# Optimization experiments

Measured on AMD Instinct MI355X. Metric: run time of the kernel, lower is better.

Reference implementation:

```python
import jax, jax.numpy as jnp
import numpy as np

B, T, D = 2, 2048, 1024
H = 4
KD = int(D * 0.5)      # total key dim = 512
VD = int(D * 1.0)      # total value dim = 1024
DK, DV = KD // H, VD // H  # per-head: 128, 256
CHUNK = 64
LOW_RANK = 16          # gate_low_rank_dim
NORMALIZER = 16.0      # gate_logit_normalizer
EPS = 1e-6


def setup_inputs() -> dict:
    key = jax.random.key(0)
    ks = jax.random.split(key, 10)
    def w(k, shape):
        return jax.random.normal(k, shape, jnp.float32) / np.sqrt(shape[0]).astype(np.float32)
    return {
        "x": jax.random.normal(ks[0], (B, T, D), jnp.float32),
        "Wq": w(ks[1], (D, KD)),
        "Wk": w(ks[2], (D, KD)),
        "Wv": w(ks[3], (D, VD)),
        "Wg": w(ks[4], (D, VD)),          # output gate projection
        "Wgk1": w(ks[5], (D, LOW_RANK)),  # low-rank gate proj (no bias)
        "Wgk2": w(ks[6], (LOW_RANK, KD)),
        "bgk2": jax.random.normal(ks[7], (KD,), jnp.float32) * 0.1,
        "gnorm_w": jnp.ones((DV,), jnp.float32),  # FusedRMSNormSwishGate weight
        "Wo": w(ks[8], (VD, D)),
    }


def reference(x, Wq, Wk, Wv, Wg, Wgk1, Wgk2, bgk2, gnorm_w, Wo):
    scale = DK ** -0.5
    NC = T // CHUNK
    # [B,T,d] -> [NC,B,H,C,d_head]
    to_heads = lambda a, d: a.reshape(B, NC, CHUNK, H, d).transpose(1, 0, 3, 2, 4)
    q = to_heads(x @ Wq, DK)
    k = to_heads(x @ Wk, DK)
    v = to_heads(x @ Wv, DV)
    # per-key log decay gate: logsigmoid(low-rank proj) / normalizer
    gk = jax.nn.log_sigmoid((x @ Wgk1) @ Wgk2 + bgk2) / NORMALIZER
    G = jnp.cumsum(to_heads(gk, DK), axis=3)  # inclusive cumsum within chunk

    def chunk_step(S, inp):
        k_c, v_c, G_c = inp                       # [B,H,C,DK],[B,H,C,DV],[B,H,C,DK]
        G_last = G_c[:, :, -1, :]                 # [B,H,DK] total chunk decay
        k_bar = k_c * jnp.exp(G_last[:, :, None, :] - G_c)  # decay pos->chunk end
        S_new = jnp.exp(G_last)[..., None] * S + jnp.einsum('bhck,bhcv->bhkv', k_bar, v_c)
        return S_new, S                           # emit state at chunk START

    S0 = jnp.zeros((B, H, DK, DV), x.dtype)
    _, S_prev = jax.lax.scan(chunk_step, S0, (k, v, G))  # [NC,B,H,DK,DV]

    qg = q * jnp.exp(G) * scale                   # decay-scaled queries
    o_inter = jnp.einsum('nbhck,nbhkv->nbhcv', qg, S_prev)
    kg = k * jnp.exp(-G)
    A = jnp.einsum('nbhik,nbhjk->nbhij', qg, kg)  # intra-chunk scores
    A = jnp.where(jnp.tril(jnp.ones((CHUNK, CHUNK), bool)), A, 0.0)
    o = o_inter + jnp.einsum('nbhij,nbhjv->nbhiv', A, v)  # [NC,B,H,C,DV]
    o = o.transpose(1, 0, 3, 2, 4).reshape(B, T, H, DV)

    # fused gated RMSNorm: rmsnorm(o)*weight * swish(g), then output proj
    g = (x @ Wg).reshape(B, T, H, DV)
    o = o * jax.lax.rsqrt(jnp.mean(o * o, axis=-1, keepdims=True) + EPS) * gnorm_w
    o = o * (g * jax.nn.sigmoid(g))
    return o.reshape(B, T, VD) @ Wo
```

## Files before the change

### kernel.cpp

```cpp
#include <hip/hip_runtime.h>
#include <hip/hip_bf16.h>

#define BDIM 2
#define TDIM 2048
#define DDIM 1024
#define HH 4
#define KD 512
#define VD 1024
#define DK 128
#define DV 256
#define NC 32
#define CHUNKC 64
#define MTOT (BDIM*TDIM)
#define QKG 1536
#define VGN 2048
#define STRIDE_ST ((size_t)BDIM*HH*DK*DV)

typedef __bf16 bf16x8 __attribute__((ext_vector_type(8)));
typedef float  f32x4  __attribute__((ext_vector_type(4)));
typedef __hip_bfloat16 hbf;

__device__ __forceinline__ void async_copy16(const void* g, void* l) {
  __builtin_amdgcn_global_load_lds(
      (const __attribute__((address_space(1))) void*)g,
      (__attribute__((address_space(3))) void*)l, 16, 0, 0);
}

__global__ void cast_bf16_kernel(const float* __restrict__ src, hbf* __restrict__ dst) {
  int t = blockIdx.x*256 + threadIdx.x;
  float4 v = ((const float4*)src)[t];
  union { hbf h[4]; uint2 u; } o;
  o.h[0] = __float2bfloat16(v.x); o.h[1] = __float2bfloat16(v.y);
  o.h[2] = __float2bfloat16(v.z); o.h[3] = __float2bfloat16(v.w);
  ((uint2*)dst)[t] = o.u;
}

__global__ void transpose_cast_kernel(const float* __restrict__ W, hbf* __restrict__ Wt,
                                      int K, int N) {
  __shared__ float tile[32][33];
  const int bx = blockIdx.x, by = blockIdx.y;
  const int tx = threadIdx.x & 31, ty = threadIdx.x >> 5;
  #pragma unroll
  for (int r = ty; r < 32; r += 8)
    tile[r][tx] = W[(size_t)(by*32 + r)*N + bx*32 + tx];
  __syncthreads();
  #pragma unroll
  for (int r = ty; r < 32; r += 8)
    Wt[(size_t)(bx*32 + r)*K + by*32 + tx] = __float2bfloat16(tile[tx][r]);
}

__global__ void wcomp_kernel(const float* __restrict__ W1, const float* __restrict__ W2,
                             hbf* __restrict__ Wct) {
  int idx = blockIdx.x*256 + threadIdx.x;
  int k = idx & 1023, n = idx >> 10;
  float s = 0.f;
  #pragma unroll
  for (int r = 0; r < 16; ++r) s += W1[k*16 + r] * W2[r*KD + n];
  Wct[(size_t)n*DDIM + k] = __float2bfloat16(s);
}

__global__ __launch_bounds__(256) void gemm_bt(const hbf* __restrict__ A,
                                               const hbf* __restrict__ Bt,
                                               float* __restrict__ C,
                                               int M, int N, int K) {
  __shared__ hbf As[128][32];
  __shared__ hbf Bs[128][32];
  const int t = threadIdx.x;
  const int w = t >> 6, l = t & 63;
  const int lr = l >> 2, lc = (l & 3)*8;
  const int lane16 = l & 15, quad = l >> 4;
  const int row0 = blockIdx.y*128, col0 = blockIdx.x*128;
  const int mb = (w >> 1)*64, nb = (w & 1)*64;

  const hbf* ga = A  + (size_t)(row0 + w*32 + lr)*K + lc;
  const hbf* gb = Bt + (size_t)(col0 + w*32 + lr)*K + lc;
  hbf* la0 = &As[w*32][0];      hbf* la1 = &As[w*32 + 16][0];
  hbf* lb0 = &Bs[w*32][0];      hbf* lb1 = &Bs[w*32 + 16][0];
  const size_t rstep = (size_t)16*K;

  f32x4 acc[4][4] = {};
  for (int k0 = 0; k0 < K; k0 += 32) {
    async_copy16(ga,         la0);
    async_copy16(ga + rstep, la1);
    async_copy16(gb,         lb0);
    async_copy16(gb + rstep, lb1);
    ga += 32; gb += 32;
    __syncthreads();
    bf16x8 af[4], bfr[4];
    #pragma unroll
    for (int i = 0; i < 4; ++i)
      af[i] = *(const bf16x8*)&As[mb + i*16 + lane16][quad*8];
    #pragma unroll
    for (int j = 0; j < 4; ++j)
      bfr[j] = *(const bf16x8*)&Bs[nb + j*16 + lane16][quad*8];
    #pragma unroll
    for (int i = 0; i < 4; ++i)
      #pragma unroll
      for (int j = 0; j < 4; ++j)
        acc[i][j] = __builtin_amdgcn_mfma_f32_16x16x32_bf16(af[i], bfr[j], acc[i][j], 0, 0, 0);
    __syncthreads();
  }
  #pragma unroll
  for (int i = 0; i < 4; ++i)
    #pragma unroll
    for (int j = 0; j < 4; ++j)
      #pragma unroll
      for (int r = 0; r < 4; ++r) {
        int m = row0 + mb + i*16 + quad*4 + r;
        int n = col0 + nb + j*16 + lane16;
        C[(size_t)m*N + n] = acc[i][j][r];
      }
}

__global__ __launch_bounds__(256) void gkcumsum_kernel(float* __restrict__ qkg,
                                                       const float* __restrict__ bias) {
  __shared__ float buf[CHUNKC][128];
  const int cs = blockIdx.x & 3;
  const int nc = (blockIdx.x >> 2) & 31;
  const int b  = blockIdx.x >> 7;
  const int t = threadIdx.x;
  const int bc = b*TDIM + nc*CHUNKC;
  const int col0 = cs*128;
  #pragma unroll
  for (int i = 0; i < 32; ++i) {
    int idx = t + 256*i;
    int c = idx >> 7, col = idx & 127;
    float s = qkg[(size_t)(bc + c)*QKG + 1024 + col0 + col] + bias[col0 + col];
    float ls = fminf(s, 0.f) - log1pf(expf(-fabsf(s)));
    buf[c][col] = ls * (1.0f/16.0f);
  }
  __syncthreads();
  if (t < 128) {
    float acc = 0.f;
    #pragma unroll
    for (int c = 0; c < CHUNKC; ++c) {
      acc += buf[c][t];
      buf[c][t] = acc;
    }
  }
  __syncthreads();
  #pragma unroll
  for (int i = 0; i < 32; ++i) {
    int idx = t + 256*i;
    int c = idx >> 7, col = idx & 127;
    qkg[(size_t)(bc + c)*QKG + 1024 + col0 + col] = buf[c][col];
  }
}

__global__ __launch_bounds__(256) void state_chunk_kernel(const float* __restrict__ qkg,
                                                          const float* __restrict__ vgb,
                                                          float* __restrict__ U,
                                                          float* __restrict__ dec) {
  const int bh = blockIdx.x & 7;
  const int nc = blockIdx.x >> 3;
  const int b = bh >> 2, h = bh & 3;
  const int t = threadIdx.x;
  const int w = t >> 6, l = t & 63;
  const int lane16 = l & 15, quad = l >> 4;
  __shared__ hbf kbarT[DK][72];
  __shared__ hbf vT[DV][72];
  __shared__ float glast[DK];
  const int bc = b*TDIM + nc*CHUNKC;
  if (t < DK) {
    float gl = qkg[(size_t)(bc + 63)*QKG + 1024 + h*DK + t];
    glast[t] = gl;
    dec[((size_t)nc*8 + bh)*DK + t] = expf(gl);
  }
  __syncthreads();
  #pragma unroll
  for (int i = 0; i < 32; ++i) {
    int idx = t + 256*i;
    int c = idx >> 7, kk = idx & 127;
    float g  = qkg[(size_t)(bc + c)*QKG + 1024 + h*DK + kk];
    float kv = qkg[(size_t)(bc + c)*QKG +  512 + h*DK + kk];
    kbarT[kk][c] = __float2bfloat16(kv * expf(glast[kk] - g));
  }
  #pragma unroll
  for (int i = 0; i < 64; ++i) {
    int idx = t + 256*i;
    int c = idx >> 8, col = idx & 255;
    vT[col][c] = __float2bfloat16(vgb[(size_t)(bc + c)*VGN + h*DV + col]);
  }
  __syncthreads();
  f32x4 acc[4][8] = {};
  #pragma unroll
  for (int kc = 0; kc < 2; ++kc) {
    bf16x8 av[4], bk[8];
    #pragma unroll
    for (int i = 0; i < 4; ++i)
      av[i] = *(const bf16x8*)&vT[w*64 + i*16 + lane16][kc*32 + quad*8];
    #pragma unroll
    for (int j = 0; j < 8; ++j)
      bk[j] = *(const bf16x8*)&kbarT[j*16 + lane16][kc*32 + quad*8];
    #pragma unroll
    for (int i = 0; i < 4; ++i)
      #pragma unroll
      for (int j = 0; j < 8; ++j)
        acc[i][j] = __builtin_amdgcn_mfma_f32_16x16x32_bf16(av[i], bk[j], acc[i][j], 0, 0, 0);
  }
  float* ub = U + ((size_t)nc*8 + bh)*((size_t)DK*DV);
  #pragma unroll
  for (int i = 0; i < 4; ++i)
    #pragma unroll
    for (int j = 0; j < 8; ++j)
      #pragma unroll
      for (int r = 0; r < 4; ++r) {
        int v = w*64 + i*16 + quad*4 + r;
        int k = j*16 + lane16;
        ub[(size_t)v*DK + k] = acc[i][j][r];
      }
}

__global__ __launch_bounds__(256) void state_scan_kernel(const float* __restrict__ U,
                                                         const float* __restrict__ dec,
                                                         hbf* __restrict__ Spb) {
  const int e = blockIdx.x*256 + threadIdx.x;
  const int k = e & 127;
  const int bh = e >> 15;
  float S = 0.f;
  for (int nc = 0; nc < NC; ++nc) {
    float u = U[(size_t)nc*STRIDE_ST + e];
    Spb[(size_t)nc*STRIDE_ST + e] = __float2bfloat16(S);
    S = S * dec[((size_t)nc*8 + bh)*DK + k] + u;
  }
}

__global__ __launch_bounds__(256) void out_kernel(const float* __restrict__ qkg,
                                                  const float* __restrict__ vgb,
                                                  const hbf* __restrict__ Spb,
                                                  const float* __restrict__ gnw,
                                                  hbf* __restrict__ obf) {
  const int blk = blockIdx.x;
  const int h = blk & 3, b = (blk >> 2) & 1, nc = blk >> 3;
  const int t = threadIdx.x;
  const int w = t >> 6, l = t & 63;
  const int lane16 = l & 15, quad = l >> 4;

  __shared__ __align__(16) unsigned char smem[64768];
  hbf (*qgs)[136] = (hbf(*)[136])(smem);
  hbf (*Ald)[72]  = (hbf(*)[72]) (smem + 17408);
  hbf (*kgs)[136] = (hbf(*)[136])(smem + 26624);
  hbf (*vT)[72]   = (hbf(*)[72]) (smem + 26624);
  float* ssum     = (float*)     (smem + 63488);
  float* invb     = (float*)     (smem + 64512);

  const float scale = 0.088388347648318447f;
  const int bc = b*TDIM + nc*CHUNKC;

  #pragma unroll
  for (int i = 0; i < 32; ++i) {
    int idx = t + 256*i;
    int c = idx >> 7, kk = idx & 127;
    size_t rb = (size_t)(bc + c)*QKG + h*DK;
    float g = qkg[rb + 1024 + (0)] ;
    g = qkg[rb + 1024 + kk - h*DK + h*DK];
    g = qkg[(size_t)(bc + c)*QKG + 1024 + h*DK + kk];
    qgs[c][kk] = __float2bfloat16(qkg[(size_t)(bc + c)*QKG + h*DK + kk] * expf(g) * scale);
    kgs[c][kk] = __float2bfloat16(qkg[(size_t)(bc + c)*QKG + 512 + h*DK + kk] * expf(-g));
  }
  __syncthreads();

  f32x4 acc1[4] = {};
  #pragma unroll
  for (int kc = 0; kc < 4; ++kc) {
    bf16x8 af = *(const bf16x8*)&qgs[w*16 + lane16][kc*32 + quad*8];
    #pragma unroll
    for (int j = 0; j < 4; ++j) {
      bf16x8 bf = *(const bf16x8*)&kgs[j*16 + lane16][kc*32 + quad*8];
      acc1[j] = __builtin_amdgcn_mfma_f32_16x16x32_bf16(af, bf, acc1[j], 0, 0, 0);
    }
  }
  __syncthreads();

  #pragma unroll
  for (int j = 0; j < 4; ++j)
    #pragma unroll
    for (int r = 0; r < 4; ++r) {
      int cr = w*16 + quad*4 + r;
      int cc = j*16 + lane16;
      Ald[cr][cc] = __float2bfloat16(cc <= cr ? acc1[j][r] : 0.f);
    }
  #pragma unroll
  for (int i = 0; i < 64; ++i) {
    int e = t + 256*i;
    int c = e >> 8, col = e & 255;
    vT[col][c] = __float2bfloat16(vgb[(size_t)(bc + c)*VGN + h*DV + col]);
  }
  __syncthreads();

  const hbf* SpB = Spb + ((size_t)nc*8 + (b*HH + h))*((size_t)DK*DV);
  f32x4 acc[4][4] = {};
  #pragma unroll
  for (int kc = 0; kc < 4; ++kc) {
    bf16x8 af[4], bs[4];
    #pragma unroll
    for (int i = 0; i < 4; ++i)
      af[i] = *(const bf16x8*)&qgs[i*16 + lane16][kc*32 + quad*8];
    #pragma unroll
    for (int j = 0; j < 4; ++j) {
      int n = w*64 + j*16 + lane16;
      bs[j] = *(const bf16x8*)(SpB + (size_t)n*DK + kc*32 + quad*8);
    }
    #pragma unroll
    for (int i = 0; i < 4; ++i)
      #pragma unroll
      for (int j = 0; j < 4; ++j)
        acc[i][j] = __builtin_amdgcn_mfma_f32_16x16x32_bf16(af[i], bs[j], acc[i][j], 0, 0, 0);
  }
  #pragma unroll
  for (int kc = 0; kc < 2; ++kc) {
    bf16x8 aa[4], bv[4];
    #pragma unroll
    for (int i = 0; i < 4; ++i)
      aa[i] = *(const bf16x8*)&Ald[i*16 + lane16][kc*32 + quad*8];
    #pragma unroll
    for (int j = 0; j < 4; ++j)
      bv[j] = *(const bf16x8*)&vT[w*64 + j*16 + lane16][kc*32 + quad*8];
    #pragma unroll
    for (int i = 0; i < 4; ++i)
      #pragma unroll
      for (int j = 0; j < 4; ++j)
        acc[i][j] = __builtin_amdgcn_mfma_f32_16x16x32_bf16(aa[i], bv[j], acc[i][j], 0, 0, 0);
  }

  #pragma unroll
  for (int i = 0; i < 4; ++i)
    #pragma unroll
    for (int r = 0; r < 4; ++r) {
      float s = 0.f;
      #pragma unroll
      for (int j = 0; j < 4; ++j) s += acc[i][j][r]*acc[i][j][r];
      s += __shfl_xor(s, 1); s += __shfl_xor(s, 2);
      s += __shfl_xor(s, 4); s += __shfl_xor(s, 8);
      if (lane16 == 0) ssum[(i*16 + quad*4 + r)*4 + w] = s;
    }
  __syncthreads();
  if (t < 64) {
    float tot = ssum[t*4] + ssum[t*4+1] + ssum[t*4+2] + ssum[t*4+3];
    invb[t] = rsqrtf(tot * (1.0f/DV) + 1e-6f);
  }
  __syncthreads();
  float gnwv[4];
  #pragma unroll
  for (int j = 0; j < 4; ++j) gnwv[j] = gnw[w*64 + j*16 + lane16];
  #pragma unroll
  for (int i = 0; i < 4; ++i)
    #pragma unroll
    for (int r = 0; r < 4; ++r) {
      int m = i*16 + quad*4 + r;
      float inv = invb[m];
      size_t grow_ = (size_t)(bc + m)*VGN + 1024 + h*DV + w*64;
      size_t orow_ = (size_t)(bc + m)*VD + h*DV + w*64;
      #pragma unroll
      for (int j = 0; j < 4; ++j) {
        float gv = vgb[grow_ + j*16 + lane16];
        float sig = 1.f / (1.f + expf(-gv));
        float val = acc[i][j][r] * inv * gnwv[j];
        obf[orow_ + j*16 + lane16] = __float2bfloat16(val * (gv * sig));
      }
    }
}

extern "C" void kernel_launch(void* const* d_in, const int* in_sizes, int n_in,
                              void* d_out, int out_size, void* d_ws, size_t ws_size,
                              hipStream_t stream) {
  const float* x    = (const float*)d_in[0];
  const float* Wq   = (const float*)d_in[1];
  const float* Wk   = (const float*)d_in[2];
  const float* Wv   = (const float*)d_in[3];
  const float* Wg   = (const float*)d_in[4];
  const float* Wgk1 = (const float*)d_in[5];
  const float* Wgk2 = (const float*)d_in[6];
  const float* bgk2 = (const float*)d_in[7];
  const float* gnw  = (const float*)d_in[8];
  const float* Wo   = (const float*)d_in[9];
  float* out = (float*)d_out;

  float* ws  = (float*)d_ws;
  float* qkg = ws;
  float* vgb = qkg + (size_t)MTOT*QKG;
  float* U   = vgb + (size_t)MTOT*VGN;
  float* dec = U   + (size_t)NC*STRIDE_ST;
  float* bfr = dec + (size_t)NC*BDIM*HH*DK;
  hbf* xbf   = (hbf*)bfr;
  hbf* wtqkg = xbf   + (size_t)MTOT*DDIM;
  hbf* wtvg  = wtqkg + (size_t)QKG*DDIM;
  hbf* wto   = wtvg  + (size_t)VGN*DDIM;
  hbf* Spb   = wto   + (size_t)DDIM*DDIM;
  hbf* obf   = (hbf*)U;

  cast_bf16_kernel<<<MTOT*DDIM/4/256, 256, 0, stream>>>(x, xbf);
  transpose_cast_kernel<<<dim3(512/32, DDIM/32), 256, 0, stream>>>(Wq, wtqkg, DDIM, 512);
  transpose_cast_kernel<<<dim3(512/32, DDIM/32), 256, 0, stream>>>(Wk, wtqkg + (size_t)512*DDIM, DDIM, 512);
  wcomp_kernel<<<512*1024/256, 256, 0, stream>>>(Wgk1, Wgk2, wtqkg + (size_t)1024*DDIM);
  transpose_cast_kernel<<<dim3(1024/32, DDIM/32), 256, 0, stream>>>(Wv, wtvg, DDIM, 1024);
  transpose_cast_kernel<<<dim3(1024/32, DDIM/32), 256, 0, stream>>>(Wg, wtvg + (size_t)1024*DDIM, DDIM, 1024);
  transpose_cast_kernel<<<dim3(1024/32, DDIM/32), 256, 0, stream>>>(Wo, wto, DDIM, 1024);

  gemm_bt<<<dim3(QKG/128, MTOT/128), 256, 0, stream>>>(xbf, wtqkg, qkg, MTOT, QKG, DDIM);
  gemm_bt<<<dim3(VGN/128, MTOT/128), 256, 0, stream>>>(xbf, wtvg, vgb, MTOT, VGN, DDIM);

  gkcumsum_kernel<<<256, 256, 0, stream>>>(qkg, bgk2);
  state_chunk_kernel<<<NC*BDIM*HH, 256, 0, stream>>>(qkg, vgb, U, dec);
  state_scan_kernel<<<(int)(STRIDE_ST/256), 256, 0, stream>>>(U, dec, Spb);
  out_kernel<<<NC*BDIM*HH, 256, 0, stream>>>(qkg, vgb, Spb, gnw, obf);
  gemm_bt<<<dim3(DDIM/128, MTOT/128), 256, 0, stream>>>(obf, wto, out, MTOT, DDIM, DDIM);
}
```

Baseline: 262.8 us.

## Merge input projection GEMMs and store q/k/v/g and chunk states in bf16

The two input projection GEMMs are merged into one launch over a concatenated weight matrix. A templated epilogue routes q/k and v/g to bf16 buffers and keeps only the gate logits in fp32. The per-chunk state contributions U are also stored in bf16, and the scan kernel processes two elements per thread with vectorized loads. This cuts global memory traffic for the intermediates and removes one launch, at the cost of extra bf16 rounding of k/v and of the state increments before accumulation.

```diff
diff --git a/kernel.cpp b/kernel.cpp
--- a/kernel.cpp
+++ b/kernel.cpp
@@ -12,8 +12,7 @@
 #define NC 32
 #define CHUNKC 64
 #define MTOT (BDIM*TDIM)
-#define QKG 1536
-#define VGN 2048
+#define NALL 3584
 #define STRIDE_ST ((size_t)BDIM*HH*DK*DV)
 
 typedef __bf16 bf16x8 __attribute__((ext_vector_type(8)));
@@ -59,9 +58,12 @@
   Wct[(size_t)n*DDIM + k] = __float2bfloat16(s);
 }
 
+template <int MODE>
 __global__ __launch_bounds__(256) void gemm_bt(const hbf* __restrict__ A,
                                                const hbf* __restrict__ Bt,
-                                               float* __restrict__ C,
+                                               float* __restrict__ Cf,
+                                               hbf* __restrict__ Cq,
+                                               hbf* __restrict__ Cv,
                                                int M, int N, int K) {
   __shared__ hbf As[128][32];
   __shared__ hbf Bs[128][32];
@@ -108,11 +110,18 @@
       for (int r = 0; r < 4; ++r) {
         int m = row0 + mb + i*16 + quad*4 + r;
         int n = col0 + nb + j*16 + lane16;
-        C[(size_t)m*N + n] = acc[i][j][r];
+        float v = acc[i][j][r];
+        if (MODE == 0) {
+          Cf[(size_t)m*N + n] = v;
+        } else {
+          if (col0 < 1024)       Cq[(size_t)m*1024 + n] = __float2bfloat16(v);
+          else if (col0 < 1536)  Cf[(size_t)m*512  + n - 1024] = v;
+          else                   Cv[(size_t)m*2048 + n - 1536] = __float2bfloat16(v);
+        }
       }
 }
 
-__global__ __launch_bounds__(256) void gkcumsum_kernel(float* __restrict__ qkg,
+__global__ __launch_bounds__(256) void gkcumsum_kernel(float* __restrict__ Gb,
                                                        const float* __restrict__ bias) {
   __shared__ float buf[CHUNKC][128];
   const int cs = blockIdx.x & 3;
@@ -125,7 +134,7 @@
   for (int i = 0; i < 32; ++i) {
     int idx = t + 256*i;
     int c = idx >> 7, col = idx & 127;
-    float s = qkg[(size_t)(bc + c)*QKG + 1024 + col0 + col] + bias[col0 + col];
+    float s = Gb[(size_t)(bc + c)*KD + col0 + col] + bias[col0 + col];
     float ls = fminf(s, 0.f) - log1pf(expf(-fabsf(s)));
     buf[c][col] = ls * (1.0f/16.0f);
   }
@@ -143,13 +152,14 @@
   for (int i = 0; i < 32; ++i) {
     int idx = t + 256*i;
     int c = idx >> 7, col = idx & 127;
-    qkg[(size_t)(bc + c)*QKG + 1024 + col0 + col] = buf[c][col];
-  }
-}
-
-__global__ __launch_bounds__(256) void state_chunk_kernel(const float* __restrict__ qkg,
-                                                          const float* __restrict__ vgb,
-                                                          float* __restrict__ U,
+    Gb[(size_t)(bc + c)*KD + col0 + col] = buf[c][col];
+  }
+}
+
+__global__ __launch_bounds__(256) void state_chunk_kernel(const hbf* __restrict__ qkbf,
+                                                          const hbf* __restrict__ vgbf,
+                                                          const float* __restrict__ Gb,
+                                                          hbf* __restrict__ Ub,
                                                           float* __restrict__ dec) {
   const int bh = blockIdx.x & 7;
   const int nc = blockIdx.x >> 3;
@@ -162,7 +172,7 @@
   __shared__ float glast[DK];
   const int bc = b*TDIM + nc*CHUNKC;
   if (t < DK) {
-    float gl = qkg[(size_t)(bc + 63)*QKG + 1024 + h*DK + t];
+    float gl = Gb[(size_t)(bc + 63)*KD + h*DK + t];
     glast[t] = gl;
     dec[((size_t)nc*8 + bh)*DK + t] = expf(gl);
   }
@@ -171,15 +181,15 @@
   for (int i = 0; i < 32; ++i) {
     int idx = t + 256*i;
     int c = idx >> 7, kk = idx & 127;
-    float g  = qkg[(size_t)(bc + c)*QKG + 1024 + h*DK + kk];
-    float kv = qkg[(size_t)(bc + c)*QKG +  512 + h*DK + kk];
+    float g  = Gb[(size_t)(bc + c)*KD + h*DK + kk];
+    float kv = __bfloat162float(qkbf[(size_t)(bc + c)*1024 + 512 + h*DK + kk]);
     kbarT[kk][c] = __float2bfloat16(kv * expf(glast[kk] - g));
   }
   #pragma unroll
   for (int i = 0; i < 64; ++i) {
     int idx = t + 256*i;
     int c = idx >> 8, col = idx & 255;
-    vT[col][c] = __float2bfloat16(vgb[(size_t)(bc + c)*VGN + h*DV + col]);
+    vT[col][c] = vgbf[(size_t)(bc + c)*2048 + h*DV + col];
   }
   __syncthreads();
   f32x4 acc[4][8] = {};
@@ -198,7 +208,7 @@
       for (int j = 0; j < 8; ++j)
         acc[i][j] = __builtin_amdgcn_mfma_f32_16x16x32_bf16(av[i], bk[j], acc[i][j], 0, 0, 0);
   }
-  float* ub = U + ((size_t)nc*8 + bh)*((size_t)DK*DV);
+  hbf* ub = Ub + ((size_t)nc*8 + bh)*((size_t)DK*DV);
   #pragma unroll
   for (int i = 0; i < 4; ++i)
     #pragma unroll
@@ -207,26 +217,35 @@
       for (int r = 0; r < 4; ++r) {
         int v = w*64 + i*16 + quad*4 + r;
         int k = j*16 + lane16;
-        ub[(size_t)v*DK + k] = acc[i][j][r];
+        ub[(size_t)v*DK + k] = __float2bfloat16(acc[i][j][r]);
       }
 }
 
-__global__ __launch_bounds__(256) void state_scan_kernel(const float* __restrict__ U,
+__global__ __launch_bounds__(256) void state_scan_kernel(const hbf* __restrict__ Ub,
                                                          const float* __restrict__ dec,
                                                          hbf* __restrict__ Spb) {
-  const int e = blockIdx.x*256 + threadIdx.x;
-  const int k = e & 127;
-  const int bh = e >> 15;
-  float S = 0.f;
+  const int p = blockIdx.x*256 + threadIdx.x;
+  const size_t e = (size_t)p*2;
+  const int k = (int)(e & 127);
+  const int bh = (int)(e >> 15);
+  float S0 = 0.f, S1 = 0.f;
   for (int nc = 0; nc < NC; ++nc) {
-    float u = U[(size_t)nc*STRIDE_ST + e];
-    Spb[(size_t)nc*STRIDE_ST + e] = __float2bfloat16(S);
-    S = S * dec[((size_t)nc*8 + bh)*DK + k] + u;
-  }
-}
-
-__global__ __launch_bounds__(256) void out_kernel(const float* __restrict__ qkg,
-                                                  const float* __restrict__ vgb,
+    const size_t off = (size_t)nc*STRIDE_ST + e;
+    uint uu = *(const uint*)(Ub + off);
+    hbf u0 = *(const hbf*)&uu;
+    hbf u1 = *((const hbf*)&uu + 1);
+    union { hbf h[2]; uint u; } ov;
+    ov.h[0] = __float2bfloat16(S0); ov.h[1] = __float2bfloat16(S1);
+    *(uint*)(Spb + off) = ov.u;
+    float2 d = *(const float2*)(dec + ((size_t)nc*8 + bh)*DK + k);
+    S0 = S0 * d.x + __bfloat162float(u0);
+    S1 = S1 * d.y + __bfloat162float(u1);
+  }
+}
+
+__global__ __launch_bounds__(256) void out_kernel(const hbf* __restrict__ qkbf,
+                                                  const hbf* __restrict__ vgbf,
+                                                  const float* __restrict__ Gb,
                                                   const hbf* __restrict__ Spb,
                                                   const float* __restrict__ gnw,
                                                   hbf* __restrict__ obf) {
@@ -251,12 +270,11 @@
   for (int i = 0; i < 32; ++i) {
     int idx = t + 256*i;
     int c = idx >> 7, kk = idx & 127;
-    size_t rb = (size_t)(bc + c)*QKG + h*DK;
-    float g = qkg[rb + 1024 + (0)] ;
-    g = qkg[rb + 1024 + kk - h*DK + h*DK];
-    g = qkg[(size_t)(bc + c)*QKG + 1024 + h*DK + kk];
-    qgs[c][kk] = __float2bfloat16(qkg[(size_t)(bc + c)*QKG + h*DK + kk] * expf(g) * scale);
-    kgs[c][kk] = __float2bfloat16(qkg[(size_t)(bc + c)*QKG + 512 + h*DK + kk] * expf(-g));
+    float g = Gb[(size_t)(bc + c)*KD + h*DK + kk];
+    float qv = __bfloat162float(qkbf[(size_t)(bc + c)*1024 + h*DK + kk]);
+    float kv = __bfloat162float(qkbf[(size_t)(bc + c)*1024 + 512 + h*DK + kk]);
+    qgs[c][kk] = __float2bfloat16(qv * expf(g) * scale);
+    kgs[c][kk] = __float2bfloat16(kv * expf(-g));
   }
   __syncthreads();
 
@@ -284,7 +302,7 @@
   for (int i = 0; i < 64; ++i) {
     int e = t + 256*i;
     int c = e >> 8, col = e & 255;
-    vT[col][c] = __float2bfloat16(vgb[(size_t)(bc + c)*VGN + h*DV + col]);
+    vT[col][c] = vgbf[(size_t)(bc + c)*2048 + h*DV + col];
   }
   __syncthreads();
 
@@ -349,11 +367,11 @@
     for (int r = 0; r < 4; ++r) {
       int m = i*16 + quad*4 + r;
       float inv = invb[m];
-      size_t grow_ = (size_t)(bc + m)*VGN + 1024 + h*DV + w*64;
+      size_t grow_ = (size_t)(bc + m)*2048 + 1024 + h*DV + w*64;
       size_t orow_ = (size_t)(bc + m)*VD + h*DV + w*64;
       #pragma unroll
       for (int j = 0; j < 4; ++j) {
-        float gv = vgb[grow_ + j*16 + lane16];
+        float gv = __bfloat162float(vgbf[grow_ + j*16 + lane16]);
         float sig = 1.f / (1.f + expf(-gv));
         float val = acc[i][j][r] * inv * gnwv[j];
         obf[orow_ + j*16 + lane16] = __float2bfloat16(val * (gv * sig));
@@ -377,32 +395,30 @@
   float* out = (float*)d_out;
 
   float* ws  = (float*)d_ws;
-  float* qkg = ws;
-  float* vgb = qkg + (size_t)MTOT*QKG;
-  float* U   = vgb + (size_t)MTOT*VGN;
-  float* dec = U   + (size_t)NC*STRIDE_ST;
-  float* bfr = dec + (size_t)NC*BDIM*HH*DK;
-  hbf* xbf   = (hbf*)bfr;
-  hbf* wtqkg = xbf   + (size_t)MTOT*DDIM;
-  hbf* wtvg  = wtqkg + (size_t)QKG*DDIM;
-  hbf* wto   = wtvg  + (size_t)VGN*DDIM;
-  hbf* Spb   = wto   + (size_t)DDIM*DDIM;
-  hbf* obf   = (hbf*)U;
+  float* Gb  = ws;
+  float* dec = Gb  + (size_t)MTOT*KD;
+  hbf* xbf   = (hbf*)(dec + (size_t)NC*BDIM*HH*DK);
+  hbf* wtall = xbf   + (size_t)MTOT*DDIM;
+  hbf* wto   = wtall + (size_t)NALL*DDIM;
+  hbf* qkbf  = wto   + (size_t)DDIM*DDIM;
+  hbf* vgbf  = qkbf  + (size_t)MTOT*1024;
+  hbf* Ub    = vgbf  + (size_t)MTOT*2048;
+  hbf* Spb   = Ub    + (size_t)NC*STRIDE_ST;
+  hbf* obf   = Ub;
 
   cast_bf16_kernel<<<MTOT*DDIM/4/256, 256, 0, stream>>>(x, xbf);
-  transpose_cast_kernel<<<dim3(512/32, DDIM/32), 256, 0, stream>>>(Wq, wtqkg, DDIM, 512);
-  transpose_cast_kernel<<<dim3(512/32, DDIM/32), 256, 0, stream>>>(Wk, wtqkg + (size_t)512*DDIM, DDIM, 512);
-  wcomp_kernel<<<512*1024/256, 256, 0, stream>>>(Wgk1, Wgk2, wtqkg + (size_t)1024*DDIM);
-  transpose_cast_kernel<<<dim3(1024/32, DDIM/32), 256, 0, stream>>>(Wv, wtvg, DDIM, 1024);
-  transpose_cast_kernel<<<dim3(1024/32, DDIM/32), 256, 0, stream>>>(Wg, wtvg + (size_t)1024*DDIM, DDIM, 1024);
+  transpose_cast_kernel<<<dim3(512/32, DDIM/32), 256, 0, stream>>>(Wq, wtall, DDIM, 512);
+  transpose_cast_kernel<<<dim3(512/32, DDIM/32), 256, 0, stream>>>(Wk, wtall + (size_t)512*DDIM, DDIM, 512);
+  wcomp_kernel<<<512*1024/256, 256, 0, stream>>>(Wgk1, Wgk2, wtall + (size_t)1024*DDIM);
+  transpose_cast_kernel<<<dim3(1024/32, DDIM/32), 256, 0, stream>>>(Wv, wtall + (size_t)1536*DDIM, DDIM, 1024);
+  transpose_cast_kernel<<<dim3(1024/32, DDIM/32), 256, 0, stream>>>(Wg, wtall + (size_t)2560*DDIM, DDIM, 1024);
   transpose_cast_kernel<<<dim3(1024/32, DDIM/32), 256, 0, stream>>>(Wo, wto, DDIM, 1024);
 
-  gemm_bt<<<dim3(QKG/128, MTOT/128), 256, 0, stream>>>(xbf, wtqkg, qkg, MTOT, QKG, DDIM);
-  gemm_bt<<<dim3(VGN/128, MTOT/128), 256, 0, stream>>>(xbf, wtvg, vgb, MTOT, VGN, DDIM);
-
-  gkcumsum_kernel<<<256, 256, 0, stream>>>(qkg, bgk2);
-  state_chunk_kernel<<<NC*BDIM*HH, 256, 0, stream>>>(qkg, vgb, U, dec);
-  state_scan_kernel<<<(int)(STRIDE_ST/256), 256, 0, stream>>>(U, dec, Spb);
-  out_kernel<<<NC*BDIM*HH, 256, 0, stream>>>(qkg, vgb, Spb, gnw, obf);
-  gemm_bt<<<dim3(DDIM/128, MTOT/128), 256, 0, stream>>>(obf, wto, out, MTOT, DDIM, DDIM);
-}
+  gemm_bt<1><<<dim3(NALL/128, MTOT/128), 256, 0, stream>>>(xbf, wtall, Gb, qkbf, vgbf, MTOT, NALL, DDIM);
+
+  gkcumsum_kernel<<<256, 256, 0, stream>>>(Gb, bgk2);
+  state_chunk_kernel<<<NC*BDIM*HH, 256, 0, stream>>>(qkbf, vgbf, Gb, Ub, dec);
+  state_scan_kernel<<<(int)(STRIDE_ST/2/256), 256, 0, stream>>>(Ub, dec, Spb);
+  out_kernel<<<NC*BDIM*HH, 256, 0, stream>>>(qkbf, vgbf, Gb, Spb, gnw, obf);
+  gemm_bt<0><<<dim3(DDIM/128, MTOT/128), 256, 0, stream>>>(obf, wto, out, (hbf*)nullptr, (hbf*)nullptr, MTOT, DDIM, DDIM);
+}
```

Measured after the change: 254.6 us. 3.1% less time.
